# Kernel tuning notes

Measured on AMD Instinct MI355X. Metric: run time of the kernel, lower is better.

The kernel has to match this reference:

```python
import jax, jax.numpy as jnp
import numpy as np

M = 4096   # out_features
N = 4096   # in_features
K_NNZ = 204  # nnz per row -> keep_ratio ~ 0.05
T = 8192   # tokens (batch*seq)


def setup_inputs() -> dict:
    key = jax.random.key(0)
    k1, k2, k3, k4 = jax.random.split(key, 4)
    # CSR structure: K_NNZ unique sorted columns per row (constant index buffers)
    rng = np.random.default_rng(0)
    cols = np.argsort(rng.random((M, N)), axis=1)[:, :K_NNZ]
    cols = np.sort(cols, axis=1).astype(np.int32)
    col_idx = jnp.asarray(cols.reshape(-1))                      # [nnz]
    row_ids = jnp.asarray(np.repeat(np.arange(M, dtype=np.int32), K_NNZ))  # [nnz]
    x = jax.random.normal(k1, (T, N), dtype=jnp.float32)
    dense_weight = jax.random.normal(k2, (M, N), dtype=jnp.float32) * 0.02
    bias = jax.random.normal(k3, (M,), dtype=jnp.float32) * 0.02
    sparse_values = jax.random.normal(k4, (M * K_NNZ,), dtype=jnp.float32) * 0.02
    return {"x": x, "dense_weight": dense_weight, "bias": bias,
            "sparse_values": sparse_values, "row_ids": row_ids, "col_idx": col_idx}


def reference(x, dense_weight, bias, sparse_values, row_ids, col_idx):
    # sp_add: scatter CSR values into the frozen dense weight (W = W_dense + W_sparse)
    W = dense_weight.at[row_ids, col_idx].add(sparse_values)     # [M, N]
    # sp_mm hot path: y = x @ W^T + b
    return jnp.dot(x, W.T) + bias                                # [T, M]
```

## Files before the change

kernel.cpp:

```cpp
#include <hip/hip_runtime.h>


typedef __attribute__((ext_vector_type(8))) __bf16 bf16x8;
typedef __attribute__((ext_vector_type(4))) float f32x4;
typedef __attribute__((ext_vector_type(8))) unsigned short u16x8;

#define BARRIER()   asm volatile("s_barrier" ::: "memory")
#define WAITLGKM(n) asm volatile("s_waitcnt lgkmcnt(" #n ")" ::: "memory")
#define WAITVM(n)   asm volatile("s_waitcnt vmcnt(" #n ")" ::: "memory")
#define SCHED0()    __builtin_amdgcn_sched_barrier(0)

__device__ __forceinline__ unsigned short f2bf(float f) {
  unsigned int u = __builtin_bit_cast(unsigned int, f);
  u += 0x7FFFu + ((u >> 16) & 1u);
  return (unsigned short)(u >> 16);
}

__global__ __launch_bounds__(256) void cvt_f32_bf16(
    const float* __restrict__ s, unsigned short* __restrict__ d, long n8) {
  long i = (long)blockIdx.x * blockDim.x + threadIdx.x;
  const long stride = (long)gridDim.x * blockDim.x;
  for (; i < n8; i += stride) {
    const float4* sp = (const float4*)(s + i * 8);
    float4 a = sp[0];
    float4 b = sp[1];
    u16x8 o;
    o[0] = f2bf(a.x); o[1] = f2bf(a.y); o[2] = f2bf(a.z); o[3] = f2bf(a.w);
    o[4] = f2bf(b.x); o[5] = f2bf(b.y); o[6] = f2bf(b.z); o[7] = f2bf(b.w);
    *(u16x8*)(d + i * 8) = o;
  }
}

__global__ __launch_bounds__(256) void sparse_scatter(
    const float* __restrict__ dense, const float* __restrict__ vals,
    const int* __restrict__ rows, const int* __restrict__ cols,
    unsigned short* __restrict__ Wb, int nnz, int K) {
  int i = blockIdx.x * blockDim.x + threadIdx.x;
  if (i < nnz) {
    size_t off = (size_t)rows[i] * (size_t)K + (size_t)cols[i];
    Wb[off] = f2bf(dense[off] + vals[i]);
  }
}

__global__ __launch_bounds__(512, 2) void gemm256(
    const unsigned short* __restrict__ A,
    const unsigned short* __restrict__ B,
    const float* __restrict__ bias,
    float* __restrict__ C,
    int Tm, int Mn, int K) {
  extern __shared__ __align__(16) char smem[];

  const int tid  = threadIdx.x;
  const int lane = tid & 63;
  const int wid  = tid >> 6;
  const int wm = (wid >> 2) * 128;
  const int wn = (wid & 3) * 64;

  const int nwg = gridDim.x;
  int bid = blockIdx.x;
  if ((nwg & 7) == 0) bid = (bid & 7) * (nwg >> 3) + (bid >> 3);
  const int ntn = Mn >> 8;
  const int bm0 = (bid / ntn) << 8;
  const int bn0 = (bid % ntn) << 8;

  const int NT = K >> 5;

  const int srow  = tid >> 2;
  const int squad = (tid & 3) ^ ((tid >> 3) & 3);
  const unsigned short* Asrc = A + (size_t)(bm0 + srow) * K + squad * 8;
  const unsigned short* Bsrc = B + (size_t)(bn0 + srow) * K + squad * 8;
  const size_t rstep = (size_t)128 * K;
  const int ldst = tid * 16;

#define STAGE(SRC, RING_OFF, KOFF) do {                                          \
    __builtin_amdgcn_global_load_lds(                                            \
        (const __attribute__((address_space(1))) void*)((SRC) + (KOFF)),         \
        (__attribute__((address_space(3))) void*)(smem + (RING_OFF) + ldst),     \
        16, 0, 0);                                                               \
    __builtin_amdgcn_global_load_lds(                                            \
        (const __attribute__((address_space(1))) void*)((SRC) + rstep + (KOFF)), \
        (__attribute__((address_space(3))) void*)(smem + (RING_OFF) + 8192 + ldst), \
        16, 0, 0);                                                               \
  } while (0)

  const int fr = lane & 15, cq = lane >> 4;
  const int roff = ((cq ^ ((fr >> 1) & 3)) << 4);
  const int aoff = (wm + fr) * 64 + roff;
  const int boff = (wn + fr) * 64 + roff;

  f32x4 acc[8][4] = {};
  bf16x8 aA[8], aB[8], b[4];

  STAGE(Asrc, 0, 0);              STAGE(Bsrc, 16384, 0);
  STAGE(Asrc, 32768, 32);         STAGE(Bsrc, 32768 + 16384, 32);
  STAGE(Asrc, 65536, 64);         STAGE(Bsrc, 65536 + 16384, 64);
  WAITVM(8);
  BARRIER();
#pragma unroll
  for (int m = 0; m < 8; ++m)
    aA[m] = *(const bf16x8*)(smem + aoff + m * 1024);

#define BODY(T, CUR, NXT) do {                                                   \
    const int t_ = (T);                                                          \
    BARRIER();                 \
    const int so_ = ((t_ + 3) & 3) * 32768;                                      \
    if (t_ + 3 < NT) {                                                           \
      const int ks_ = (t_ + 3) * 32;                                             \
      STAGE(Asrc, so_, ks_);                                                     \
      STAGE(Bsrc, so_ + 16384, ks_);                                             \
      WAITVM(8);                    \
    } else if (t_ + 2 < NT) { WAITVM(4); }                                       \
    else if (t_ + 1 < NT)   { WAITVM(0); }                                       \
    BARRIER();                             \
    {                                                                            \
      const char* Br_ = smem + (t_ & 3) * 32768 + 16384;                         \
      _Pragma("unroll")                                                          \
      for (int n = 0; n < 4; ++n)                                                \
        b[n] = *(const bf16x8*)(Br_ + boff + n * 1024);                          \
    }                                                                            \
    SCHED0();                   \
    if (t_ + 1 < NT) {                                                           \
      const char* An_ = smem + ((t_ + 1) & 3) * 32768;                           \
      _Pragma("unroll")                                                          \
      for (int m = 0; m < 8; ++m)                                                \
        NXT[m] = *(const bf16x8*)(An_ + aoff + m * 1024);                        \
      WAITLGKM(8);            \
    } else {                                                                     \
      WAITLGKM(0);                                                               \
    }                                                                            \
    SCHED0();                                                                    \
    __builtin_amdgcn_s_setprio(1);                                               \
    _Pragma("unroll")                                                            \
    for (int m = 0; m < 8; ++m)                                                  \
      _Pragma("unroll")                                                          \
      for (int n = 0; n < 4; ++n)                                                \
        acc[m][n] = __builtin_amdgcn_mfma_f32_16x16x32_bf16(CUR[m], b[n],        \
                                                            acc[m][n], 0, 0, 0);\
    __builtin_amdgcn_s_setprio(0);                                               \
  } while (0)

  for (int t = 0; t < NT; t += 2) {
    BODY(t,     aA, aB);
    BODY(t + 1, aB, aA);
  }
#undef BODY
#undef STAGE

  const int c4 = cq * 4;
#pragma unroll
  for (int n = 0; n < 4; ++n) {
    const int col = bn0 + wn + n * 16 + fr;
    const float bv = bias[col];
#pragma unroll
    for (int m = 0; m < 8; ++m) {
      const size_t rowb = (size_t)(bm0 + wm + m * 16 + c4);
#pragma unroll
      for (int q = 0; q < 4; ++q)
        C[(rowb + q) * (size_t)Mn + col] = acc[m][n][q] + bv;
    }
  }
}

extern "C" void kernel_launch(void* const* d_in, const int* in_sizes, int n_in,
                              void* d_out, int out_size, void* d_ws, size_t ws_size,
                              hipStream_t stream) {
  const float* x     = (const float*)d_in[0];
  const float* dw    = (const float*)d_in[1];
  const float* bias  = (const float*)d_in[2];
  const float* sv    = (const float*)d_in[3];
  const int*   rows  = (const int*)d_in[4];
  const int*   cols  = (const int*)d_in[5];
  float* out = (float*)d_out;

  const int  Mn = in_sizes[2];
  const long wElems = (long)in_sizes[1];
  const int  K  = (int)(wElems / Mn);
  const long xElems = (long)in_sizes[0];
  const int  Tm = (int)(xElems / K);
  const int  nnz = in_sizes[3];

  unsigned short* Wb = (unsigned short*)d_ws;
  unsigned short* Xb = Wb + wElems;

  cvt_f32_bf16<<<2048, 256, 0, stream>>>(dw, Wb, wElems / 8);
  sparse_scatter<<<(nnz + 255) / 256, 256, 0, stream>>>(dw, sv, rows, cols, Wb, nnz, K);
  cvt_f32_bf16<<<2048, 256, 0, stream>>>(x, Xb, xElems / 8);

  dim3 grid((Tm >> 8) * (Mn >> 8));
  gemm256<<<grid, 512, 131072, stream>>>(Xb, Wb, bias, out, Tm, Mn, K);
}
```

Baseline: 328.9 us.

## Load A fragments directly from global into registers, stage only B via LDS

The A (activation) tile no longer goes through shared memory. Each wave now loads its own A fragments straight from global memory into registers, one K-step ahead. Only B is staged through a 4-deep LDS ring, which halves LDS use from 128 KB to 64 KB and drops one of the two barriers per iteration. The trade-off is that A reads lose cross-wave reuse, since waves in the same block re-read overlapping rows. The per-thread global loads are also 16-byte strided rows, which may be less coalesced and expose global latency to the MFMA loop.

```diff
diff --git a/kernel.cpp b/kernel.cpp
--- a/kernel.cpp
+++ b/kernel.cpp
@@ -67,67 +67,58 @@
 
   const int srow  = tid >> 2;
   const int squad = (tid & 3) ^ ((tid >> 3) & 3);
-  const unsigned short* Asrc = A + (size_t)(bm0 + srow) * K + squad * 8;
   const unsigned short* Bsrc = B + (size_t)(bn0 + srow) * K + squad * 8;
   const size_t rstep = (size_t)128 * K;
   const int ldst = tid * 16;
 
-#define STAGE(SRC, RING_OFF, KOFF) do {                                          \
+#define STAGE(RING_OFF, KOFF) do {                                               \
     __builtin_amdgcn_global_load_lds(                                            \
-        (const __attribute__((address_space(1))) void*)((SRC) + (KOFF)),         \
+        (const __attribute__((address_space(1))) void*)(Bsrc + (KOFF)),          \
         (__attribute__((address_space(3))) void*)(smem + (RING_OFF) + ldst),     \
         16, 0, 0);                                                               \
     __builtin_amdgcn_global_load_lds(                                            \
-        (const __attribute__((address_space(1))) void*)((SRC) + rstep + (KOFF)), \
+        (const __attribute__((address_space(1))) void*)(Bsrc + rstep + (KOFF)),  \
         (__attribute__((address_space(3))) void*)(smem + (RING_OFF) + 8192 + ldst), \
         16, 0, 0);                                                               \
   } while (0)
 
   const int fr = lane & 15, cq = lane >> 4;
-  const int roff = ((cq ^ ((fr >> 1) & 3)) << 4);
-  const int aoff = (wm + fr) * 64 + roff;
-  const int boff = (wn + fr) * 64 + roff;
+  const int boff = (wn + fr) * 64 + ((cq ^ ((fr >> 1) & 3)) << 4);
+
+  const unsigned short* Afrag = A + (size_t)(bm0 + wm + fr) * K + cq * 8;
+  const size_t mstride = (size_t)16 * K;
 
   f32x4 acc[8][4] = {};
   bf16x8 aA[8], aB[8], b[4];
 
-  STAGE(Asrc, 0, 0);              STAGE(Bsrc, 16384, 0);
-  STAGE(Asrc, 32768, 32);         STAGE(Bsrc, 32768 + 16384, 32);
-  STAGE(Asrc, 65536, 64);         STAGE(Bsrc, 65536 + 16384, 64);
+  STAGE(0, 0);
+  STAGE(16384, 32);
+  STAGE(32768, 64);
+#pragma unroll
+  for (int m = 0; m < 8; ++m)
+    aA[m] = *(const bf16x8*)(Afrag + m * mstride);
   WAITVM(8);
   BARRIER();
-#pragma unroll
-  for (int m = 0; m < 8; ++m)
-    aA[m] = *(const bf16x8*)(smem + aoff + m * 1024);
 
 #define BODY(T, CUR, NXT) do {                                                   \
     const int t_ = (T);                                                          \
-    BARRIER();                 \
-    const int so_ = ((t_ + 3) & 3) * 32768;                                      \
-    if (t_ + 3 < NT) {                                                           \
-      const int ks_ = (t_ + 3) * 32;                                             \
-      STAGE(Asrc, so_, ks_);                                                     \
-      STAGE(Bsrc, so_ + 16384, ks_);                                             \
-      WAITVM(8);                    \
-    } else if (t_ + 2 < NT) { WAITVM(4); }                                       \
-    else if (t_ + 1 < NT)   { WAITVM(0); }                                       \
-    BARRIER();                             \
+    if (t_ + 3 < NT) STAGE(((t_ + 3) & 3) * 16384, (t_ + 3) * 32);               \
+    if (t_ + 1 < NT) {                                                           \
+      const size_t ko_ = (size_t)(t_ + 1) * 32;                                  \
+      _Pragma("unroll")                                                          \
+      for (int m = 0; m < 8; ++m)                                                \
+        NXT[m] = *(const bf16x8*)(Afrag + m * mstride + ko_);                    \
+    }                                                                            \
+    if (t_ + 3 < NT)      { WAITVM(10); }                                        \
+    else if (t_ + 1 < NT) { WAITVM(8); }                                         \
+    else                  { WAITVM(0); }                                         \
     {                                                                            \
-      const char* Br_ = smem + (t_ & 3) * 32768 + 16384;                         \
+      const char* Br_ = smem + (t_ & 3) * 16384;                                 \
       _Pragma("unroll")                                                          \
       for (int n = 0; n < 4; ++n)                                                \
         b[n] = *(const bf16x8*)(Br_ + boff + n * 1024);                          \
     }                                                                            \
-    SCHED0();                   \
-    if (t_ + 1 < NT) {                                                           \
-      const char* An_ = smem + ((t_ + 1) & 3) * 32768;                           \
-      _Pragma("unroll")                                                          \
-      for (int m = 0; m < 8; ++m)                                                \
-        NXT[m] = *(const bf16x8*)(An_ + aoff + m * 1024);                        \
-      WAITLGKM(8);            \
-    } else {                                                                     \
-      WAITLGKM(0);                                                               \
-    }                                                                            \
+    WAITLGKM(0);                                                                 \
     SCHED0();                                                                    \
     __builtin_amdgcn_s_setprio(1);                                               \
     _Pragma("unroll")                                                            \
@@ -137,6 +128,7 @@
         acc[m][n] = __builtin_amdgcn_mfma_f32_16x16x32_bf16(CUR[m], b[n],        \
                                                             acc[m][n], 0, 0, 0);\
     __builtin_amdgcn_s_setprio(0);                                               \
+    BARRIER();                                                                   \
   } while (0)
 
   for (int t = 0; t < NT; t += 2) {
@@ -187,5 +179,5 @@
   cvt_f32_bf16<<<2048, 256, 0, stream>>>(x, Xb, xElems / 8);
 
   dim3 grid((Tm >> 8) * (Mn >> 8));
-  gemm256<<<grid, 512, 131072, stream>>>(Xb, Wb, bias, out, Tm, Mn, K);
+  gemm256<<<grid, 512, 65536, stream>>>(Xb, Wb, bias, out, Tm, Mn, K);
 }
```

After: 678.9 us. 106% more time.
